# Kernel optimization log

Measured on AMD Instinct MI355X. Metric: run time of the kernel, lower is better.

Reference implementation:

```python
import jax, jax.numpy as jnp
import numpy as np

E, D, H, K, N = 8, 512, 2048, 2, 1024  # experts, d_model, d_hidden, top_k, tokens
EPS = 1e-5


def _moe_linear(x, idx, W, b):
    # x: (M, in); idx: (M,) expert id per row; W: (E, out, in); b: (E, out)
    # Brute-force: compute per-expert dense GEMMs, select via one-hot (matches
    # BruteForceMoELinear math: y[i] = x[i] @ W[idx[i]].T + b[idx[i]]).
    m = jax.nn.one_hot(idx, W.shape[0], dtype=x.dtype)  # (M, E)
    y = jnp.einsum('me,eoi,mi->mo', m, W, x)
    return y + jnp.take(b, idx, axis=0)


def _forward(inp, gate_w, gate_b, w1, b1, w2, b2, ln_w, ln_b):
    # NaiveGate: linear -> top_k -> softmax over top-k logits
    logits = inp @ gate_w.T + gate_b              # (N, E)
    top_val, top_idx = jax.lax.top_k(logits, K)   # (N, K)
    score = jax.nn.softmax(top_val, axis=-1)      # (N, K)
    # repeat_interleave tokens, dispatch to experts
    x = jnp.repeat(inp, K, axis=0)                # (N*K, D)
    idx = top_idx.reshape(-1)                     # (N*K,)
    x = _moe_linear(x, idx, w1, b1)               # (N*K, H)
    x = jax.nn.gelu(x, approximate=False)         # torch F.gelu default = erf
    x = _moe_linear(x, idx, w2, b2)               # (N*K, D)
    x = x.reshape(N, K, D)
    x = jnp.einsum('nk,nkd->nd', score, x)        # bmm((N,1,K),(N,K,D)) combine
    # post layer norm (pre_lnorm=False)
    mu = jnp.mean(x, axis=-1, keepdims=True)
    var = jnp.var(x, axis=-1, keepdims=True)
    return (x - mu) * jax.lax.rsqrt(var + EPS) * ln_w + ln_b


def setup_inputs() -> dict:
    key = jax.random.key(0)
    ks = jax.random.split(key, 8)
    s = 0.02
    return {
        'inp': jax.random.normal(ks[0], (N, D), dtype=jnp.float32),
        'gate_w': s * jax.random.normal(ks[1], (E, D), dtype=jnp.float32),
        'gate_b': jnp.zeros((E,), dtype=jnp.float32),
        'w1': s * jax.random.normal(ks[2], (E, H, D), dtype=jnp.float32),
        'b1': jnp.zeros((E, H), dtype=jnp.float32),
        'w2': s * jax.random.normal(ks[3], (E, D, H), dtype=jnp.float32),
        'b2': jnp.zeros((E, D), dtype=jnp.float32),
        'ln_w': jnp.ones((D,), dtype=jnp.float32),
        'ln_b': jnp.zeros((D,), dtype=jnp.float32),
    }


def reference(inp, gate_w, gate_b, w1, b1, w2, b2, ln_w, ln_b):
    return _forward(inp, gate_w, gate_b, w1, b1, w2, b2, ln_w, ln_b)
```

## Files before the change

kernel.cpp:

```cpp
#include <hip/hip_runtime.h>
#include <cstdint>
#include <cstddef>

typedef _Float16 half_t;
typedef _Float16 half8 __attribute__((ext_vector_type(8)));
typedef float floatx4 __attribute__((ext_vector_type(4)));

#define E_ 8
#define D_ 512
#define H_ 2048
#define NTOK 1024
#define NP 2048
#define TM 64
#define MAX_TILES 40

__device__ __forceinline__ float gelu_f(float x) {
    return 0.5f * x * (1.0f + erff(x * 0.7071067811865476f));
}

__device__ __forceinline__ half8 cvt8(floatx4 a, floatx4 b) {
    half8 h = { (half_t)a[0], (half_t)a[1], (half_t)a[2], (half_t)a[3],
                (half_t)b[0], (half_t)b[1], (half_t)b[2], (half_t)b[3] };
    return h;
}

__global__ __launch_bounds__(256) void gate_kernel(
        const float* __restrict__ inp, const float* __restrict__ gate_w,
        const float* __restrict__ gate_b, float* __restrict__ logits) {
    int n = blockIdx.x * 4 + (threadIdx.x >> 6);
    int lane = threadIdx.x & 63;
    const floatx4* xr = (const floatx4*)(inp + (size_t)n * D_);
    floatx4 x0 = xr[lane * 2], x1 = xr[lane * 2 + 1];
    #pragma unroll
    for (int e = 0; e < E_; e++) {
        const floatx4* gr = (const floatx4*)(gate_w + (size_t)e * D_);
        floatx4 g0 = gr[lane * 2], g1 = gr[lane * 2 + 1];
        float p = x0[0]*g0[0] + x0[1]*g0[1] + x0[2]*g0[2] + x0[3]*g0[3]
                + x1[0]*g1[0] + x1[1]*g1[1] + x1[2]*g1[2] + x1[3]*g1[3];
        #pragma unroll
        for (int m = 1; m < 64; m <<= 1) p += __shfl_xor(p, m);
        if (lane == 0) logits[(size_t)n * E_ + e] = p + gate_b[e];
    }
}

__global__ __launch_bounds__(256) void plan_kernel(
        const float* __restrict__ logits, float* __restrict__ score,
        int* __restrict__ idx, int* __restrict__ pos_of_pair,
        int* __restrict__ tok_of_pos,
        int* __restrict__ tile_e, int* __restrict__ tile_row0,
        int* __restrict__ tile_cnt, int* __restrict__ ntiles) {
    __shared__ int cnt_s[E_], off_s[E_ + 1], cur_s[E_];
    int tid = threadIdx.x;
    if (tid < E_) { cnt_s[tid] = 0; cur_s[tid] = 0; }
    __syncthreads();
    int my_e[4][2];
    #pragma unroll
    for (int i = 0; i < 4; i++) {
        int n = tid + i * 256;
        float l[E_];
        #pragma unroll
        for (int e = 0; e < E_; e++) l[e] = logits[(size_t)n * E_ + e];
        int e0 = 0; float v0 = l[0];
        #pragma unroll
        for (int e = 1; e < E_; e++) if (l[e] > v0) { v0 = l[e]; e0 = e; }
        int e1 = -1; float v1 = -3.4e38f;
        #pragma unroll
        for (int e = 0; e < E_; e++) if (e != e0 && l[e] > v1) { v1 = l[e]; e1 = e; }
        float s1 = expf(v1 - v0);
        float den = 1.0f + s1;
        score[2 * n]     = 1.0f / den;
        score[2 * n + 1] = s1 / den;
        idx[2 * n]     = e0;
        idx[2 * n + 1] = e1;
        atomicAdd(&cnt_s[e0], 1);
        atomicAdd(&cnt_s[e1], 1);
        my_e[i][0] = e0; my_e[i][1] = e1;
    }
    __syncthreads();
    if (tid == 0) {
        int o = 0;
        #pragma unroll
        for (int e = 0; e < E_; e++) { off_s[e] = o; o += cnt_s[e]; }
        off_s[E_] = o;
        int t = 0;
        for (int e = 0; e < E_; e++) {
            int c = cnt_s[e];
            int nt = (c + TM - 1) / TM;
            for (int i = 0; i < nt; i++) {
                tile_e[t] = e;
                tile_row0[t] = off_s[e] + i * TM;
                int rem = c - i * TM;
                tile_cnt[t] = rem < TM ? rem : TM;
                t++;
            }
        }
        ntiles[0] = t;
    }
    __syncthreads();
    #pragma unroll
    for (int i = 0; i < 4; i++) {
        #pragma unroll
        for (int k = 0; k < 2; k++) {
            int pp = (tid + i * 256) * 2 + k;
            int e = my_e[i][k];
            int r = atomicAdd(&cur_s[e], 1);
            int pos = off_s[e] + r;
            pos_of_pair[pp] = pos;
            tok_of_pos[pos] = pp >> 1;
        }
    }
}

__global__ __launch_bounds__(256) void gemm1_kernel(
        const float* __restrict__ inp, const int* __restrict__ tok_of_pos,
        const float* __restrict__ w1, const float* __restrict__ b1,
        const int* __restrict__ tile_e, const int* __restrict__ tile_row0,
        const int* __restrict__ tile_cnt, const int* __restrict__ ntiles,
        half_t* __restrict__ Y1) {
    __shared__ half_t Bs[64 * 512];
    __shared__ half_t As[2][64 * 64];
    const int bid = blockIdx.x, tid = threadIdx.x;
    const int xcd = bid & 7, ib = bid >> 3;
    const int t = ib % MAX_TILES;
    const int cb = xcd * 4 + ib / MAX_TILES;
    if (t >= ntiles[0]) return;
    const int e = tile_e[t], row0 = tile_row0[t], cnt = tile_cnt[t];
    const int colbase = cb * 64;
    const int wave = tid >> 6, lane = tid & 63;
    const int quad = lane >> 4, l16 = lane & 15;
    const int wm = (wave & 1) * 32, wn = (wave >> 1) * 32;
    const int xm = l16 & 7;

    const int gr0 = tid >> 3, gr1 = gr0 + 32, gc = tid & 7;
    const int sw0 = gc ^ (gr0 & 7), sw1 = gc ^ (gr1 & 7);
    const int sa0 = gr0 * 64 + sw0 * 8, sa1 = gr1 * 64 + sw1 * 8;
    int ar0 = row0 + gr0; if (ar0 > NP - 1) ar0 = NP - 1;
    int ar1 = row0 + gr1; if (ar1 > NP - 1) ar1 = NP - 1;
    const floatx4* Ag0 = (const floatx4*)(inp + (size_t)tok_of_pos[ar0] * D_) + gc * 2;
    const floatx4* Ag1 = (const floatx4*)(inp + (size_t)tok_of_pos[ar1] * D_) + gc * 2;

    floatx4 ra0a, ra0b, ra1a, ra1b;
    #define LOADA(kq) do { \
        ra0a = Ag0[kq]; ra0b = Ag0[(kq) + 1]; \
        ra1a = Ag1[kq]; ra1b = Ag1[(kq) + 1]; } while (0)
    #define CVWA(buf) do { \
        *(half8*)(&As[buf][sa0]) = cvt8(ra0a, ra0b); \
        *(half8*)(&As[buf][sa1]) = cvt8(ra1a, ra1b); } while (0)

    LOADA(0);

    #pragma unroll
    for (int hb = 0; hb < 2; hb++) {
        floatx4 v0[8], v1[8];
        #pragma unroll
        for (int u = 0; u < 8; u++) {
            int gid = tid + (hb * 8 + u) * 256;
            int row = gid >> 6, g = gid & 63;
            const floatx4* src = (const floatx4*)(w1 + ((size_t)e * H_ + colbase + row) * D_ + g * 8);
            v0[u] = src[0]; v1[u] = src[1];
        }
        #pragma unroll
        for (int u = 0; u < 8; u++) {
            int gid = tid + (hb * 8 + u) * 256;
            int row = gid >> 6, g = gid & 63;
            int gs = (g & 56) | ((g ^ row) & 7);
            *(half8*)(&Bs[row * 512 + gs * 8]) = cvt8(v0[u], v1[u]);
        }
    }
    CVWA(0);
    __syncthreads();

    floatx4 acc[2][2] = {};
    int cur = 0;
    for (int k0 = 0; k0 < D_; k0 += 64) {
        bool more = (k0 + 64) < D_;
        if (more) LOADA((k0 + 64) >> 2);
        const half_t* Ab = &As[cur][0];
        const int kg0 = k0 >> 3;
        #pragma unroll
        for (int ks = 0; ks < 2; ks++) {
            half8 a[2], b[2];
            #pragma unroll
            for (int mi = 0; mi < 2; mi++)
                a[mi] = *(const half8*)(Ab + (wm + mi * 16 + l16) * 64 + ((ks * 4 + quad) ^ xm) * 8);
            #pragma unroll
            for (int ni = 0; ni < 2; ni++)
                b[ni] = *(const half8*)(&Bs[(wn + ni * 16 + l16) * 512 + (kg0 + ((ks * 4 + quad) ^ xm)) * 8]);
            #pragma unroll
            for (int mi = 0; mi < 2; mi++)
                #pragma unroll
                for (int ni = 0; ni < 2; ni++)
                    acc[mi][ni] = __builtin_amdgcn_mfma_f32_16x16x32_f16(a[mi], b[ni], acc[mi][ni], 0, 0, 0);
        }
        if (more) CVWA(cur ^ 1);
        __syncthreads();
        cur ^= 1;
    }
    #undef LOADA
    #undef CVWA

    float bias[2];
    #pragma unroll
    for (int ni = 0; ni < 2; ni++)
        bias[ni] = b1[(size_t)e * H_ + colbase + wn + ni * 16 + l16];
    #pragma unroll
    for (int mi = 0; mi < 2; mi++) {
        #pragma unroll
        for (int r = 0; r < 4; r++) {
            int rr = wm + mi * 16 + quad * 4 + r;
            if (rr >= cnt) continue;
            size_t rowoff = (size_t)(row0 + rr) * H_;
            #pragma unroll
            for (int ni = 0; ni < 2; ni++) {
                float v = acc[mi][ni][r] + bias[ni];
                Y1[rowoff + colbase + wn + ni * 16 + l16] = (half_t)gelu_f(v);
            }
        }
    }
}

__global__ __launch_bounds__(256) void gemm2_kernel(
        const half_t* __restrict__ Y1, const float* __restrict__ w2,
        const int* __restrict__ tile_e, const int* __restrict__ tile_row0,
        const int* __restrict__ tile_cnt, const int* __restrict__ ntiles,
        float* __restrict__ Y2p) {
    __shared__ half_t Bs[64 * 512];
    __shared__ half_t As[2][64 * 64];
    const int bid = blockIdx.x, tid = threadIdx.x;
    const int xcd = bid & 7, ib = bid >> 3;
    const int t = ib % MAX_TILES;
    const int kz = ib / MAX_TILES;
    if (t >= ntiles[0]) return;
    const int e = tile_e[t], row0 = tile_row0[t], cnt = tile_cnt[t];
    const int colbase = xcd * 64;
    const int kzbase = kz * 512;
    const int wave = tid >> 6, lane = tid & 63;
    const int quad = lane >> 4, l16 = lane & 15;
    const int wm = (wave & 1) * 32, wn = (wave >> 1) * 32;
    const int xm = l16 & 7;

    const int gr0 = tid >> 3, gr1 = gr0 + 32, gc = tid & 7;
    const int sw0 = gc ^ (gr0 & 7), sw1 = gc ^ (gr1 & 7);
    const int sa0 = gr0 * 64 + sw0 * 8, sa1 = gr1 * 64 + sw1 * 8;
    const half8* Ag0 = (const half8*)(Y1 + (size_t)(row0 + gr0) * H_ + kzbase) + gc;
    const half8* Ag1 = (const half8*)(Y1 + (size_t)(row0 + gr1) * H_ + kzbase) + gc;

    half8 ha0, ha1;
    #define LOADA2(k0) do { \
        ha0 = Ag0[(k0) >> 3]; ha1 = Ag1[(k0) >> 3]; } while (0)
    #define CVWA2(buf) do { \
        *(half8*)(&As[buf][sa0]) = ha0; \
        *(half8*)(&As[buf][sa1]) = ha1; } while (0)

    LOADA2(0);

    #pragma unroll
    for (int hb = 0; hb < 2; hb++) {
        floatx4 v0[8], v1[8];
        #pragma unroll
        for (int u = 0; u < 8; u++) {
            int gid = tid + (hb * 8 + u) * 256;
            int row = gid >> 6, g = gid & 63;
            const floatx4* src = (const floatx4*)(w2 + ((size_t)e * D_ + colbase + row) * H_ + kzbase + g * 8);
            v0[u] = src[0]; v1[u] = src[1];
        }
        #pragma unroll
        for (int u = 0; u < 8; u++) {
            int gid = tid + (hb * 8 + u) * 256;
            int row = gid >> 6, g = gid & 63;
            int gs = (g & 56) | ((g ^ row) & 7);
            *(half8*)(&Bs[row * 512 + gs * 8]) = cvt8(v0[u], v1[u]);
        }
    }
    CVWA2(0);
    __syncthreads();

    floatx4 acc[2][2] = {};
    int cur = 0;
    for (int k0 = 0; k0 < 512; k0 += 64) {
        bool more = (k0 + 64) < 512;
        if (more) LOADA2(k0 + 64);
        const half_t* Ab = &As[cur][0];
        const int kg0 = k0 >> 3;
        #pragma unroll
        for (int ks = 0; ks < 2; ks++) {
            half8 a[2], b[2];
            #pragma unroll
            for (int mi = 0; mi < 2; mi++)
                a[mi] = *(const half8*)(Ab + (wm + mi * 16 + l16) * 64 + ((ks * 4 + quad) ^ xm) * 8);
            #pragma unroll
            for (int ni = 0; ni < 2; ni++)
                b[ni] = *(const half8*)(&Bs[(wn + ni * 16 + l16) * 512 + (kg0 + ((ks * 4 + quad) ^ xm)) * 8]);
            #pragma unroll
            for (int mi = 0; mi < 2; mi++)
                #pragma unroll
                for (int ni = 0; ni < 2; ni++)
                    acc[mi][ni] = __builtin_amdgcn_mfma_f32_16x16x32_f16(a[mi], b[ni], acc[mi][ni], 0, 0, 0);
        }
        if (more) CVWA2(cur ^ 1);
        __syncthreads();
        cur ^= 1;
    }
    #undef LOADA2
    #undef CVWA2

    #pragma unroll
    for (int mi = 0; mi < 2; mi++) {
        #pragma unroll
        for (int r = 0; r < 4; r++) {
            int rr = wm + mi * 16 + quad * 4 + r;
            if (rr >= cnt) continue;
            size_t rowoff = ((size_t)kz * NP + row0 + rr) * D_;
            #pragma unroll
            for (int ni = 0; ni < 2; ni++)
                Y2p[rowoff + colbase + wn + ni * 16 + l16] = acc[mi][ni][r];
        }
    }
}

__global__ __launch_bounds__(256) void final_kernel(
        const float* __restrict__ Y2p, const float* __restrict__ b2,
        const int* __restrict__ idx, const float* __restrict__ score,
        const int* __restrict__ pos_of_pair,
        const float* __restrict__ ln_w, const float* __restrict__ ln_b,
        float* __restrict__ out) {
    int n = blockIdx.x * 4 + (threadIdx.x >> 6);
    int lane = threadIdx.x & 63;
    int p0 = pos_of_pair[2 * n], p1 = pos_of_pair[2 * n + 1];
    int e0 = idx[2 * n], e1 = idx[2 * n + 1];
    float s0 = score[2 * n], s1 = score[2 * n + 1];

    const floatx4* b2r0 = (const floatx4*)(b2 + (size_t)e0 * D_);
    const floatx4* b2r1 = (const floatx4*)(b2 + (size_t)e1 * D_);
    floatx4 a_lo = b2r0[lane * 2], a_hi = b2r0[lane * 2 + 1];
    floatx4 c_lo = b2r1[lane * 2], c_hi = b2r1[lane * 2 + 1];
    #pragma unroll
    for (int kz = 0; kz < 4; kz++) {
        const floatx4* r0 = (const floatx4*)(Y2p + ((size_t)kz * NP + p0) * D_);
        const floatx4* r1 = (const floatx4*)(Y2p + ((size_t)kz * NP + p1) * D_);
        a_lo += r0[lane * 2]; a_hi += r0[lane * 2 + 1];
        c_lo += r1[lane * 2]; c_hi += r1[lane * 2 + 1];
    }
    floatx4 y_lo = s0 * a_lo + s1 * c_lo;
    floatx4 y_hi = s0 * a_hi + s1 * c_hi;

    float s = 0.0f, q = 0.0f;
    #pragma unroll
    for (int j = 0; j < 4; j++) {
        s += y_lo[j] + y_hi[j];
        q += y_lo[j] * y_lo[j] + y_hi[j] * y_hi[j];
    }
    #pragma unroll
    for (int m = 1; m < 64; m <<= 1) {
        s += __shfl_xor(s, m);
        q += __shfl_xor(q, m);
    }
    float mean = s * (1.0f / 512.0f);
    float var = q * (1.0f / 512.0f) - mean * mean;
    float inv = 1.0f / sqrtf(var + 1e-5f);

    const floatx4* wv = (const floatx4*)ln_w;
    const floatx4* bv = (const floatx4*)ln_b;
    floatx4 o_lo = (y_lo - mean) * inv * wv[lane * 2]     + bv[lane * 2];
    floatx4 o_hi = (y_hi - mean) * inv * wv[lane * 2 + 1] + bv[lane * 2 + 1];
    floatx4* op = (floatx4*)(out + (size_t)n * D_);
    op[lane * 2] = o_lo;
    op[lane * 2 + 1] = o_hi;
}

extern "C" void kernel_launch(void* const* d_in, const int* in_sizes, int n_in,
                              void* d_out, int out_size, void* d_ws, size_t ws_size,
                              hipStream_t stream) {
    const float* inp    = (const float*)d_in[0];
    const float* gate_w = (const float*)d_in[1];
    const float* gate_b = (const float*)d_in[2];
    const float* w1     = (const float*)d_in[3];
    const float* b1     = (const float*)d_in[4];
    const float* w2     = (const float*)d_in[5];
    const float* b2     = (const float*)d_in[6];
    const float* ln_w   = (const float*)d_in[7];
    const float* ln_b   = (const float*)d_in[8];
    float* out = (float*)d_out;

    char* ws = (char*)d_ws;
    size_t o = 0;
    auto carve = [&](size_t bytes) -> char* {
        char* p = ws + o;
        o += (bytes + 255) & ~(size_t)255;
        return p;
    };
    half_t* Y1  = (half_t*)carve(sizeof(half_t) * (size_t)(NP + 128) * H_);
    float*  Y2p = (float*)carve(sizeof(float) * 4 * (size_t)NP * D_);
    float*  logits = (float*)carve(sizeof(float) * NTOK * E_);
    float*  score  = (float*)carve(sizeof(float) * NP);
    int* idx         = (int*)carve(sizeof(int) * NP);
    int* pos_of_pair = (int*)carve(sizeof(int) * NP);
    int* tok_of_pos  = (int*)carve(sizeof(int) * NP);
    int* tile_e      = (int*)carve(sizeof(int) * MAX_TILES);
    int* tile_row0   = (int*)carve(sizeof(int) * MAX_TILES);
    int* tile_cnt    = (int*)carve(sizeof(int) * MAX_TILES);
    int* ntiles      = (int*)carve(sizeof(int) * 1);

    gate_kernel<<<NTOK / 4, 256, 0, stream>>>(inp, gate_w, gate_b, logits);
    plan_kernel<<<1, 256, 0, stream>>>(logits, score, idx, pos_of_pair, tok_of_pos,
                                       tile_e, tile_row0, tile_cnt, ntiles);
    gemm1_kernel<<<MAX_TILES * 32, 256, 0, stream>>>(
        inp, tok_of_pos, w1, b1, tile_e, tile_row0, tile_cnt, ntiles, Y1);
    gemm2_kernel<<<MAX_TILES * 32, 256, 0, stream>>>(
        Y1, w2, tile_e, tile_row0, tile_cnt, ntiles, Y2p);
    final_kernel<<<NTOK / 4, 256, 0, stream>>>(Y2p, b2, idx, score, pos_of_pair, ln_w, ln_b, out);
}
```

Before: 177.1 us.

## Drop LDS staging in MoE GEMMs and load MFMA operands directly from global

Both expert GEMM kernels stop staging A and B tiles in shared memory with swizzled layouts and double buffering. Each lane now reads its MFMA fragments straight from global memory and converts fp32 to fp16 in registers. GEMM1 widens the column tile to 128 per block, and GEMM2 halves the split-K factor from 4 to 2, which shrinks the partial-sum buffer and the reduction work in the final kernel. This removes LDS traffic and barriers, but the loads become strided and uncoalesced, data is no longer reused across waves, and there is no prefetch to hide global latency.

```diff
diff --git a/kernel.cpp b/kernel.cpp
--- a/kernel.cpp
+++ b/kernel.cpp
@@ -117,91 +117,56 @@
         const int* __restrict__ tile_e, const int* __restrict__ tile_row0,
         const int* __restrict__ tile_cnt, const int* __restrict__ ntiles,
         half_t* __restrict__ Y1) {
-    __shared__ half_t Bs[64 * 512];
-    __shared__ half_t As[2][64 * 64];
-    const int bid = blockIdx.x, tid = threadIdx.x;
-    const int xcd = bid & 7, ib = bid >> 3;
-    const int t = ib % MAX_TILES;
-    const int cb = xcd * 4 + ib / MAX_TILES;
+    const int t = blockIdx.x;
     if (t >= ntiles[0]) return;
     const int e = tile_e[t], row0 = tile_row0[t], cnt = tile_cnt[t];
-    const int colbase = cb * 64;
+    const int colbase = blockIdx.y * 128;
+    const int tid = threadIdx.x;
     const int wave = tid >> 6, lane = tid & 63;
     const int quad = lane >> 4, l16 = lane & 15;
-    const int wm = (wave & 1) * 32, wn = (wave >> 1) * 32;
-    const int xm = l16 & 7;
-
-    const int gr0 = tid >> 3, gr1 = gr0 + 32, gc = tid & 7;
-    const int sw0 = gc ^ (gr0 & 7), sw1 = gc ^ (gr1 & 7);
-    const int sa0 = gr0 * 64 + sw0 * 8, sa1 = gr1 * 64 + sw1 * 8;
-    int ar0 = row0 + gr0; if (ar0 > NP - 1) ar0 = NP - 1;
-    int ar1 = row0 + gr1; if (ar1 > NP - 1) ar1 = NP - 1;
-    const floatx4* Ag0 = (const floatx4*)(inp + (size_t)tok_of_pos[ar0] * D_) + gc * 2;
-    const floatx4* Ag1 = (const floatx4*)(inp + (size_t)tok_of_pos[ar1] * D_) + gc * 2;
-
-    floatx4 ra0a, ra0b, ra1a, ra1b;
-    #define LOADA(kq) do { \
-        ra0a = Ag0[kq]; ra0b = Ag0[(kq) + 1]; \
-        ra1a = Ag1[kq]; ra1b = Ag1[(kq) + 1]; } while (0)
-    #define CVWA(buf) do { \
-        *(half8*)(&As[buf][sa0]) = cvt8(ra0a, ra0b); \
-        *(half8*)(&As[buf][sa1]) = cvt8(ra1a, ra1b); } while (0)
-
-    LOADA(0);
-
-    #pragma unroll
-    for (int hb = 0; hb < 2; hb++) {
-        floatx4 v0[8], v1[8];
-        #pragma unroll
-        for (int u = 0; u < 8; u++) {
-            int gid = tid + (hb * 8 + u) * 256;
-            int row = gid >> 6, g = gid & 63;
-            const floatx4* src = (const floatx4*)(w1 + ((size_t)e * H_ + colbase + row) * D_ + g * 8);
-            v0[u] = src[0]; v1[u] = src[1];
-        }
-        #pragma unroll
-        for (int u = 0; u < 8; u++) {
-            int gid = tid + (hb * 8 + u) * 256;
-            int row = gid >> 6, g = gid & 63;
-            int gs = (g & 56) | ((g ^ row) & 7);
-            *(half8*)(&Bs[row * 512 + gs * 8]) = cvt8(v0[u], v1[u]);
-        }
-    }
-    CVWA(0);
-    __syncthreads();
-
-    floatx4 acc[2][2] = {};
-    int cur = 0;
+    const int wm = (wave & 1) * 32, wn = (wave >> 1) * 64;
+
+    const float* ap[2];
+    #pragma unroll
+    for (int mi = 0; mi < 2; mi++) {
+        int ar = row0 + wm + mi * 16 + l16;
+        if (ar > NP - 1) ar = NP - 1;
+        ap[mi] = inp + (size_t)tok_of_pos[ar] * D_ + quad * 8;
+    }
+    const float* bp[4];
+    #pragma unroll
+    for (int ni = 0; ni < 4; ni++)
+        bp[ni] = w1 + ((size_t)e * H_ + colbase + wn + ni * 16 + l16) * D_ + quad * 8;
+
+    floatx4 acc[2][4] = {};
     for (int k0 = 0; k0 < D_; k0 += 64) {
-        bool more = (k0 + 64) < D_;
-        if (more) LOADA((k0 + 64) >> 2);
-        const half_t* Ab = &As[cur][0];
-        const int kg0 = k0 >> 3;
-        #pragma unroll
-        for (int ks = 0; ks < 2; ks++) {
-            half8 a[2], b[2];
-            #pragma unroll
-            for (int mi = 0; mi < 2; mi++)
-                a[mi] = *(const half8*)(Ab + (wm + mi * 16 + l16) * 64 + ((ks * 4 + quad) ^ xm) * 8);
-            #pragma unroll
-            for (int ni = 0; ni < 2; ni++)
-                b[ni] = *(const half8*)(&Bs[(wn + ni * 16 + l16) * 512 + (kg0 + ((ks * 4 + quad) ^ xm)) * 8]);
+        half8 ah[2][2];
+        #pragma unroll
+        for (int mi = 0; mi < 2; mi++)
+            #pragma unroll
+            for (int ks = 0; ks < 2; ks++) {
+                const floatx4* pa = (const floatx4*)(ap[mi] + k0 + ks * 32);
+                ah[mi][ks] = cvt8(pa[0], pa[1]);
+            }
+        #pragma unroll
+        for (int ni = 0; ni < 4; ni++) {
+            half8 bh[2];
+            #pragma unroll
+            for (int ks = 0; ks < 2; ks++) {
+                const floatx4* pb = (const floatx4*)(bp[ni] + k0 + ks * 32);
+                bh[ks] = cvt8(pb[0], pb[1]);
+            }
             #pragma unroll
             for (int mi = 0; mi < 2; mi++)
                 #pragma unroll
-                for (int ni = 0; ni < 2; ni++)
-                    acc[mi][ni] = __builtin_amdgcn_mfma_f32_16x16x32_f16(a[mi], b[ni], acc[mi][ni], 0, 0, 0);
-        }
-        if (more) CVWA(cur ^ 1);
-        __syncthreads();
-        cur ^= 1;
-    }
-    #undef LOADA
-    #undef CVWA
-
-    float bias[2];
-    #pragma unroll
-    for (int ni = 0; ni < 2; ni++)
+                for (int ks = 0; ks < 2; ks++)
+                    acc[mi][ni] = __builtin_amdgcn_mfma_f32_16x16x32_f16(ah[mi][ks], bh[ks], acc[mi][ni], 0, 0, 0);
+        }
+    }
+
+    float bias[4];
+    #pragma unroll
+    for (int ni = 0; ni < 4; ni++)
         bias[ni] = b1[(size_t)e * H_ + colbase + wn + ni * 16 + l16];
     #pragma unroll
     for (int mi = 0; mi < 2; mi++) {
@@ -211,7 +176,7 @@
             if (rr >= cnt) continue;
             size_t rowoff = (size_t)(row0 + rr) * H_;
             #pragma unroll
-            for (int ni = 0; ni < 2; ni++) {
+            for (int ni = 0; ni < 4; ni++) {
                 float v = acc[mi][ni][r] + bias[ni];
                 Y1[rowoff + colbase + wn + ni * 16 + l16] = (half_t)gelu_f(v);
             }
@@ -224,85 +189,49 @@
         const int* __restrict__ tile_e, const int* __restrict__ tile_row0,
         const int* __restrict__ tile_cnt, const int* __restrict__ ntiles,
         float* __restrict__ Y2p) {
-    __shared__ half_t Bs[64 * 512];
-    __shared__ half_t As[2][64 * 64];
-    const int bid = blockIdx.x, tid = threadIdx.x;
-    const int xcd = bid & 7, ib = bid >> 3;
-    const int t = ib % MAX_TILES;
-    const int kz = ib / MAX_TILES;
+    const int t = blockIdx.x;
     if (t >= ntiles[0]) return;
     const int e = tile_e[t], row0 = tile_row0[t], cnt = tile_cnt[t];
-    const int colbase = xcd * 64;
-    const int kzbase = kz * 512;
+    const int colbase = blockIdx.y * 64;
+    const int kz = blockIdx.z;
+    const int kzbase = kz * 1024;
+    const int tid = threadIdx.x;
     const int wave = tid >> 6, lane = tid & 63;
     const int quad = lane >> 4, l16 = lane & 15;
     const int wm = (wave & 1) * 32, wn = (wave >> 1) * 32;
-    const int xm = l16 & 7;
-
-    const int gr0 = tid >> 3, gr1 = gr0 + 32, gc = tid & 7;
-    const int sw0 = gc ^ (gr0 & 7), sw1 = gc ^ (gr1 & 7);
-    const int sa0 = gr0 * 64 + sw0 * 8, sa1 = gr1 * 64 + sw1 * 8;
-    const half8* Ag0 = (const half8*)(Y1 + (size_t)(row0 + gr0) * H_ + kzbase) + gc;
-    const half8* Ag1 = (const half8*)(Y1 + (size_t)(row0 + gr1) * H_ + kzbase) + gc;
-
-    half8 ha0, ha1;
-    #define LOADA2(k0) do { \
-        ha0 = Ag0[(k0) >> 3]; ha1 = Ag1[(k0) >> 3]; } while (0)
-    #define CVWA2(buf) do { \
-        *(half8*)(&As[buf][sa0]) = ha0; \
-        *(half8*)(&As[buf][sa1]) = ha1; } while (0)
-
-    LOADA2(0);
-
-    #pragma unroll
-    for (int hb = 0; hb < 2; hb++) {
-        floatx4 v0[8], v1[8];
-        #pragma unroll
-        for (int u = 0; u < 8; u++) {
-            int gid = tid + (hb * 8 + u) * 256;
-            int row = gid >> 6, g = gid & 63;
-            const floatx4* src = (const floatx4*)(w2 + ((size_t)e * D_ + colbase + row) * H_ + kzbase + g * 8);
-            v0[u] = src[0]; v1[u] = src[1];
-        }
-        #pragma unroll
-        for (int u = 0; u < 8; u++) {
-            int gid = tid + (hb * 8 + u) * 256;
-            int row = gid >> 6, g = gid & 63;
-            int gs = (g & 56) | ((g ^ row) & 7);
-            *(half8*)(&Bs[row * 512 + gs * 8]) = cvt8(v0[u], v1[u]);
-        }
-    }
-    CVWA2(0);
-    __syncthreads();
+
+    const half_t* ap[2];
+    #pragma unroll
+    for (int mi = 0; mi < 2; mi++)
+        ap[mi] = Y1 + (size_t)(row0 + wm + mi * 16 + l16) * H_ + kzbase + quad * 8;
+    const float* bp[2];
+    #pragma unroll
+    for (int ni = 0; ni < 2; ni++)
+        bp[ni] = w2 + ((size_t)e * D_ + colbase + wn + ni * 16 + l16) * H_ + kzbase + quad * 8;
 
     floatx4 acc[2][2] = {};
-    int cur = 0;
-    for (int k0 = 0; k0 < 512; k0 += 64) {
-        bool more = (k0 + 64) < 512;
-        if (more) LOADA2(k0 + 64);
-        const half_t* Ab = &As[cur][0];
-        const int kg0 = k0 >> 3;
-        #pragma unroll
-        for (int ks = 0; ks < 2; ks++) {
-            half8 a[2], b[2];
-            #pragma unroll
-            for (int mi = 0; mi < 2; mi++)
-                a[mi] = *(const half8*)(Ab + (wm + mi * 16 + l16) * 64 + ((ks * 4 + quad) ^ xm) * 8);
-            #pragma unroll
-            for (int ni = 0; ni < 2; ni++)
-                b[ni] = *(const half8*)(&Bs[(wn + ni * 16 + l16) * 512 + (kg0 + ((ks * 4 + quad) ^ xm)) * 8]);
+    for (int k0 = 0; k0 < 1024; k0 += 64) {
+        half8 ah[2][2];
+        #pragma unroll
+        for (int mi = 0; mi < 2; mi++)
+            #pragma unroll
+            for (int ks = 0; ks < 2; ks++)
+                ah[mi][ks] = *(const half8*)(ap[mi] + k0 + ks * 32);
+        #pragma unroll
+        for (int ni = 0; ni < 2; ni++) {
+            half8 bh[2];
+            #pragma unroll
+            for (int ks = 0; ks < 2; ks++) {
+                const floatx4* pb = (const floatx4*)(bp[ni] + k0 + ks * 32);
+                bh[ks] = cvt8(pb[0], pb[1]);
+            }
             #pragma unroll
             for (int mi = 0; mi < 2; mi++)
                 #pragma unroll
-                for (int ni = 0; ni < 2; ni++)
-                    acc[mi][ni] = __builtin_amdgcn_mfma_f32_16x16x32_f16(a[mi], b[ni], acc[mi][ni], 0, 0, 0);
-        }
-        if (more) CVWA2(cur ^ 1);
-        __syncthreads();
-        cur ^= 1;
-    }
-    #undef LOADA2
-    #undef CVWA2
+                for (int ks = 0; ks < 2; ks++)
+                    acc[mi][ni] = __builtin_amdgcn_mfma_f32_16x16x32_f16(ah[mi][ks], bh[ks], acc[mi][ni], 0, 0, 0);
+        }
+    }
 
     #pragma unroll
     for (int mi = 0; mi < 2; mi++) {
@@ -335,7 +264,7 @@
     floatx4 a_lo = b2r0[lane * 2], a_hi = b2r0[lane * 2 + 1];
     floatx4 c_lo = b2r1[lane * 2], c_hi = b2r1[lane * 2 + 1];
     #pragma unroll
-    for (int kz = 0; kz < 4; kz++) {
+    for (int kz = 0; kz < 2; kz++) {
         const floatx4* r0 = (const floatx4*)(Y2p + ((size_t)kz * NP + p0) * D_);
         const floatx4* r1 = (const floatx4*)(Y2p + ((size_t)kz * NP + p1) * D_);
         a_lo += r0[lane * 2]; a_hi += r0[lane * 2 + 1];
@@ -390,7 +319,7 @@
         return p;
     };
     half_t* Y1  = (half_t*)carve(sizeof(half_t) * (size_t)(NP + 128) * H_);
-    float*  Y2p = (float*)carve(sizeof(float) * 4 * (size_t)NP * D_);
+    float*  Y2p = (float*)carve(sizeof(float) * 2 * (size_t)NP * D_);
     float*  logits = (float*)carve(sizeof(float) * NTOK * E_);
     float*  score  = (float*)carve(sizeof(float) * NP);
     int* idx         = (int*)carve(sizeof(int) * NP);
@@ -404,9 +333,9 @@
     gate_kernel<<<NTOK / 4, 256, 0, stream>>>(inp, gate_w, gate_b, logits);
     plan_kernel<<<1, 256, 0, stream>>>(logits, score, idx, pos_of_pair, tok_of_pos,
                                        tile_e, tile_row0, tile_cnt, ntiles);
-    gemm1_kernel<<<MAX_TILES * 32, 256, 0, stream>>>(
+    gemm1_kernel<<<dim3(MAX_TILES, H_ / 128), 256, 0, stream>>>(
         inp, tok_of_pos, w1, b1, tile_e, tile_row0, tile_cnt, ntiles, Y1);
-    gemm2_kernel<<<MAX_TILES * 32, 256, 0, stream>>>(
+    gemm2_kernel<<<dim3(MAX_TILES, D_ / 64, 2), 256, 0, stream>>>(
         Y1, w2, tile_e, tile_row0, tile_cnt, ntiles, Y2p);
     final_kernel<<<NTOK / 4, 256, 0, stream>>>(Y2p, b2, idx, score, pos_of_pair, ln_w, ln_b, out);
 }
```

Result: slower. 251.2 us (+41.8%).
